# Kernel optimization log

Hardware: AMD Instinct MI355X
Metric: run time of the kernel (lower is better)

The kernel has to match this reference:

```python
import jax, jax.numpy as jnp
import numpy as np

C = 256
NH = 8
STRIDE = 4
HD = C // NH
SCALE = HD ** -0.5


def conv2d(x, w, b, stride=1, padding='VALID', groups=1):
    y = jax.lax.conv_general_dilated(
        x, w, (stride, stride), padding,
        dimension_numbers=('NCHW', 'OIHW', 'NCHW'),
        feature_group_count=groups)
    return y + b[None, :, None, None]


def setup_inputs() -> dict:
    key = jax.random.key(0)
    ks = jax.random.split(key, 20)
    s = 0.02
    d = {
        'x': jax.random.normal(ks[0], (8, C, 64, 64), jnp.float32),
        'wq': jax.random.normal(ks[1], (2 * C, C, 1, 1), jnp.float32) * s,
        'bq': jnp.zeros((2 * C,), jnp.float32),
        'ws': jax.random.normal(ks[2], (C, C, STRIDE, STRIDE), jnp.float32) * s,
        'bs': jnp.zeros((C,), jnp.float32),
        'wak_d': jax.random.normal(ks[3], (C, 1, 3, 3), jnp.float32) * s,
        'bak_d': jnp.zeros((C,), jnp.float32),
        'wak_p': jax.random.normal(ks[4], (C, C, 1, 1), jnp.float32) * s,
        'bak_p': jnp.zeros((C,), jnp.float32),
        'wav_d': jax.random.normal(ks[5], (C, 1, 3, 3), jnp.float32) * s,
        'bav_d': jnp.zeros((C,), jnp.float32),
        'wav_p': jax.random.normal(ks[6], (C, C, 1, 1), jnp.float32) * s,
        'bav_p': jnp.zeros((C,), jnp.float32),
        'wek': jax.random.normal(ks[7], (C, C, 1, 1), jnp.float32) * s,
        'bek': jnp.zeros((C,), jnp.float32),
        'wev': jax.random.normal(ks[8], (C, C, 1, 1), jnp.float32) * s,
        'bev': jnp.zeros((C,), jnp.float32),
        'wproj': jax.random.normal(ks[9], (C, 2 * C, 1, 1), jnp.float32) * s,
        'bproj': jnp.zeros((C,), jnp.float32),
    }
    return d


def _heads_kv(t):
    # [B,C,h,w] -> [B,NH,N_kv,HD]
    B = t.shape[0]
    return t.reshape(B, NH, HD, -1).transpose(0, 1, 3, 2)


def _attn_branch(q, k, v):
    # q: [B,NH,Nq,HD], k/v: [B,NH,Nkv,HD]
    attn = jnp.einsum('bhqd,bhkd->bhqk', q, k) * SCALE
    attn = jax.nn.softmax(attn, axis=-1)
    return jnp.einsum('bhqk,bhkd->bhqd', attn, v)


def reference(x, wq, bq, ws, bs, wak_d, bak_d, wak_p, bak_p,
              wav_d, bav_d, wav_p, bav_p, wek, bek, wev, bev, wproj, bproj):
    B, Cc, H, W = x.shape
    # QKV-style 1x1 query projection -> two query sets
    q = conv2d(x, wq, bq)  # [B,2C,H,W]
    q = q.reshape(B, 2, NH, HD, H * W).transpose(1, 0, 2, 4, 3)  # [2,B,NH,HW,HD]
    qa, qe = q[0], q[1]
    # spatial reduction
    xr = conv2d(x, ws, bs, stride=STRIDE)  # [B,C,H/s,W/s]
    spak = _heads_kv(conv2d(conv2d(xr, wak_d, bak_d, padding=[(1, 1), (1, 1)], groups=C), wak_p, bak_p))
    spav = _heads_kv(conv2d(conv2d(xr, wav_d, bav_d, padding=[(1, 1), (1, 1)], groups=C), wav_p, bav_p))
    spek = _heads_kv(conv2d(xr, wek, bek))
    spev = _heads_kv(conv2d(xr, wev, bev))
    outa = _attn_branch(qa, spak, spav).transpose(0, 1, 3, 2).reshape(B, Cc, H, W)
    oute = _attn_branch(qe, spek, spev).transpose(0, 1, 3, 2).reshape(B, Cc, H, W)
    out = jnp.concatenate((outa, oute), axis=1)
    return conv2d(out, wproj, bproj)
```

## Files before the change

### kernel.cpp

```cpp
#include <hip/hip_runtime.h>
#include <hip/hip_bf16.h>

#define QSC (0.17677669529663687f * 1.4426950408889634f)

typedef __attribute__((ext_vector_type(8))) short bf16x8;
typedef __attribute__((ext_vector_type(4))) float f32x4;
typedef unsigned short u16;

union FragU { unsigned u[4]; uint4 q; bf16x8 v; };

__device__ inline u16 f2bu(float a) {
  union { __hip_bfloat16 h; u16 s; } c;
  c.h = __float2bfloat16(a);
  return c.s;
}
__device__ inline unsigned pk2(float lo, float hi) {
  unsigned r;
  asm("v_cvt_pk_bf16_f32 %0, %1, %2" : "=v"(r) : "v"(lo), "v"(hi));
  return r;
}
__device__ inline float exp2r(float x) {
  float r;
  asm("v_exp_f32 %0, %1" : "=v"(r) : "v"(x));
  return r;
}
__device__ inline void gl16(const u16* g, u16* l) {
  __builtin_amdgcn_global_load_lds(
      (const __attribute__((address_space(1))) unsigned int*)g,
      (__attribute__((address_space(3))) unsigned int*)l, 16, 0, 0);
}
__device__ inline void waitvm0() {
  asm volatile("s_waitcnt vmcnt(0)" ::: "memory");
}

__global__ __launch_bounds__(256) void k_xT(
    const float* __restrict__ X, u16* __restrict__ XT,
    const float* __restrict__ wq, const float* __restrict__ wproj,
    const float* __restrict__ ws,
    const float* __restrict__ w0, const float* __restrict__ w1,
    const float* __restrict__ w2, const float* __restrict__ w3,
    u16* __restrict__ wqb, u16* __restrict__ wpb,
    u16* __restrict__ wsb, u16* __restrict__ wkvb) {
  if (blockIdx.z == 8) {
    int which = blockIdx.y;
    int tid = blockIdx.x * 256 + threadIdx.x;
    const int ST = 16384;
    if (which == 0) {
      for (int i = tid; i < 131072; i += ST) wqb[i] = f2bu(wq[i]);
    } else if (which == 1) {
      for (int i = tid; i < 131072; i += ST) wpb[i] = f2bu(wproj[i]);
    } else if (which == 2) {
      for (int i = tid; i < 1048576; i += ST) {
        int co = i >> 12, rem = i & 4095, tap = rem >> 8, ci = rem & 255;
        wsb[i] = f2bu(ws[co * 4096 + ci * 16 + tap]);
      }
    } else if (which < 7) {
      const float* src = (which == 3) ? w0 : (which == 4) ? w1 : (which == 5) ? w2 : w3;
      u16* dst = wkvb + (size_t)(which - 3) * 65536;
      for (int i = tid; i < 65536; i += ST) dst[i] = f2bu(src[i]);
    }
    return;
  }
  __shared__ float L[32 * 65];
  int n0 = blockIdx.x * 64, c0 = blockIdx.y * 32, b = blockIdx.z;
  int t = threadIdx.x;
#pragma unroll
  for (int i = 0; i < 8; ++i) {
    int idx = i * 256 + t;
    int r = idx >> 6, nn = idx & 63;
    L[r * 65 + nn] = X[((size_t)(b * 256 + c0 + r)) * 4096 + n0 + nn];
  }
  __syncthreads();
  int nn = t >> 2, cq = t & 3;
  uint4 u;
  u.x = pk2(L[(cq * 8 + 0) * 65 + nn], L[(cq * 8 + 1) * 65 + nn]);
  u.y = pk2(L[(cq * 8 + 2) * 65 + nn], L[(cq * 8 + 3) * 65 + nn]);
  u.z = pk2(L[(cq * 8 + 4) * 65 + nn], L[(cq * 8 + 5) * 65 + nn]);
  u.w = pk2(L[(cq * 8 + 6) * 65 + nn], L[(cq * 8 + 7) * 65 + nn]);
  *(uint4*)(XT + ((size_t)b * 4096 + n0 + nn) * 256 + c0 + cq * 8) = u;
}

__global__ __launch_bounds__(256) void k_gemm_qproj(
    const u16* __restrict__ XT, const u16* __restrict__ Wb,
    const float* __restrict__ bias, u16* __restrict__ Qb) {
  __shared__ __align__(16) u16 SM[16384];
  int n0 = blockIdx.x * 128, m0 = blockIdx.y * 128, b = blockIdx.z;
  int t = threadIdx.x, w = t >> 6, l = t & 63, g = l >> 4, lq = l & 15;
  int wr = w >> 1, wc = w & 1;
  const u16* Xb = XT + (size_t)b * 4096 * 256;
  int srow = w * 32 + (l >> 2), scol = (l & 3) * 8;
  const u16* gA = Wb + (size_t)(m0 + srow) * 256 + scol;
  const u16* gB = Xb + (size_t)(n0 + srow) * 256 + scol;
  u16* lA = SM + w * 1024;
  u16* lB = SM + 8192 + w * 1024;

  f32x4 acc[4][4];
#pragma unroll
  for (int ms = 0; ms < 4; ++ms)
#pragma unroll
    for (int ns = 0; ns < 4; ++ns) acc[ms][ns] = {0.f, 0.f, 0.f, 0.f};

  gl16(gA, lA); gl16(gA + 16 * 256, lA + 512);
  gl16(gB, lB); gl16(gB + 16 * 256, lB + 512);
  waitvm0();
  __syncthreads();
#pragma unroll
  for (int kt = 0; kt < 8; ++kt) {
    int cur = kt & 1;
    if (kt < 7) {
      int sel = cur ^ 1, ko = (kt + 1) * 32;
      gl16(gA + ko, lA + sel * 4096); gl16(gA + 16 * 256 + ko, lA + sel * 4096 + 512);
      gl16(gB + ko, lB + sel * 4096); gl16(gB + 16 * 256 + ko, lB + sel * 4096 + 512);
    }
    const u16* Ab = SM + cur * 4096;
    const u16* Bb = SM + 8192 + cur * 4096;
    FragU a[4], bb[4];
#pragma unroll
    for (int ms = 0; ms < 4; ++ms)
      a[ms].q = *(const uint4*)(Ab + (wr * 64 + ms * 16 + lq) * 32 + g * 8);
#pragma unroll
    for (int ns = 0; ns < 4; ++ns)
      bb[ns].q = *(const uint4*)(Bb + (wc * 64 + ns * 16 + lq) * 32 + g * 8);
#pragma unroll
    for (int ms = 0; ms < 4; ++ms)
#pragma unroll
      for (int ns = 0; ns < 4; ++ns)
        acc[ms][ns] = __builtin_amdgcn_mfma_f32_16x16x32_bf16(a[ms].v, bb[ns].v, acc[ms][ns], 0, 0, 0);
    waitvm0();
    __syncthreads();
  }

  float bR[4][4];
#pragma unroll
  for (int ms = 0; ms < 4; ++ms)
#pragma unroll
    for (int r = 0; r < 4; ++r) bR[ms][r] = bias[m0 + wr * 64 + ms * 16 + g * 4 + r];

  char* Lc = (char*)SM;
#pragma unroll
  for (int ms = 0; ms < 4; ++ms)
#pragma unroll
    for (int ns = 0; ns < 4; ++ns) {
      int nl = wc * 64 + ns * 16 + lq;
      int mb2 = (wr * 64 + ms * 16 + g * 4) * 2;
      int off = (nl * 256 + mb2) ^ ((nl & 7) << 4);
      *(uint2*)(Lc + off) = make_uint2(
          pk2((acc[ms][ns][0] + bR[ms][0]) * QSC, (acc[ms][ns][1] + bR[ms][1]) * QSC),
          pk2((acc[ms][ns][2] + bR[ms][2]) * QSC, (acc[ms][ns][3] + bR[ms][3]) * QSC));
    }
  __syncthreads();
  int sh0 = m0 >> 5;
#pragma unroll
  for (int rr = 0; rr < 8; ++rr) {
    int idx = rr * 256 + t;
    int ch = idx & 3, shl = (idx >> 2) & 3, nn = idx >> 4;
    int off = (nn * 256 + shl * 64 + ch * 16) ^ ((nn & 7) << 4);
    uint4 v = *(const uint4*)(Lc + off);
    *(uint4*)(Qb + ((size_t)(b * 16 + sh0 + shl) * 4096 + n0 + nn) * 32 + ch * 8) = v;
  }
}

__global__ __launch_bounds__(256) void k_gemm_sr(
    const u16* __restrict__ XT, const u16* __restrict__ Wb,
    float* __restrict__ Psr) {
  __shared__ __align__(16) u16 SM[16384];
  int ks = blockIdx.x, b = blockIdx.z;
  int m0 = (blockIdx.y >> 1) * 128, n0 = (blockIdx.y & 1) * 128;
  int t = threadIdx.x, w = t >> 6, l = t & 63, g = l >> 4, lq = l & 15;
  int wr = w >> 1, wc = w & 1;
  const u16* Xb = XT + (size_t)b * 4096 * 256;
  int srow = w * 32 + (l >> 2), scol = (l & 3) * 8;
  const u16* gA = Wb + (size_t)(m0 + srow) * 4096 + scol;
  u16* lA = SM + w * 1024;
  u16* lB = SM + 8192 + w * 1024;
  int nA = n0 + srow, nB = nA + 16;
  int iA = nA >> 4, jA = nA & 15, iB = nB >> 4, jB = nB & 15;

  f32x4 acc[4][4];
#pragma unroll
  for (int ms = 0; ms < 4; ++ms)
#pragma unroll
    for (int ns = 0; ns < 4; ++ns) acc[ms][ns] = {0.f, 0.f, 0.f, 0.f};

#define SR_STAGE(sel, kt) {                                                   \
    int ktg = ks * 16 + (kt);                                                 \
    int tap = ktg >> 3, ci0 = (ktg & 7) * 32;                                 \
    int ky = tap >> 2, kx = tap & 3;                                          \
    gl16(gA + ktg * 32, lA + (sel) * 4096);                                   \
    gl16(gA + (size_t)16 * 4096 + ktg * 32, lA + (sel) * 4096 + 512);         \
    int pixA = (4 * iA + ky) * 64 + 4 * jA + kx;                              \
    int pixB = (4 * iB + ky) * 64 + 4 * jB + kx;                              \
    gl16(Xb + (size_t)pixA * 256 + ci0 + scol, lB + (sel) * 4096);            \
    gl16(Xb + (size_t)pixB * 256 + ci0 + scol, lB + (sel) * 4096 + 512); }

  SR_STAGE(0, 0);
  waitvm0();
  __syncthreads();
#pragma unroll
  for (int kt = 0; kt < 16; ++kt) {
    int cur = kt & 1;
    if (kt < 15) SR_STAGE(cur ^ 1, kt + 1);
    const u16* Ab = SM + cur * 4096;
    const u16* Bb = SM + 8192 + cur * 4096;
    FragU a[4], bb[4];
#pragma unroll
    for (int ms = 0; ms < 4; ++ms)
      a[ms].q = *(const uint4*)(Ab + (wr * 64 + ms * 16 + lq) * 32 + g * 8);
#pragma unroll
    for (int ns = 0; ns < 4; ++ns)
      bb[ns].q = *(const uint4*)(Bb + (wc * 64 + ns * 16 + lq) * 32 + g * 8);
#pragma unroll
    for (int ms = 0; ms < 4; ++ms)
#pragma unroll
      for (int ns = 0; ns < 4; ++ns)
        acc[ms][ns] = __builtin_amdgcn_mfma_f32_16x16x32_bf16(a[ms].v, bb[ns].v, acc[ms][ns], 0, 0, 0);
    waitvm0();
    __syncthreads();
  }
#undef SR_STAGE
#pragma unroll
  for (int ms = 0; ms < 4; ++ms)
#pragma unroll
    for (int ns = 0; ns < 4; ++ns) {
      int n = n0 + wc * 64 + ns * 16 + lq;
#pragma unroll
      for (int r = 0; r < 4; ++r) {
        int m = m0 + wr * 64 + ms * 16 + g * 4 + r;
        Psr[(((size_t)ks * 8 + b) * 256 + m) * 256 + n] = acc[ms][ns][r];
      }
    }
}

__global__ __launch_bounds__(256) void k_srdw(
    const float* __restrict__ Psr, const float* __restrict__ bias,
    const float* __restrict__ wkd, const float* __restrict__ bkd,
    const float* __restrict__ wvd, const float* __restrict__ bvd,
    u16* __restrict__ xrT, u16* __restrict__ TKt, u16* __restrict__ TVt) {
  __shared__ float L[32 * 256];
  int cg = blockIdx.x, b = blockIdx.y, t = threadIdx.x;
#pragma unroll
  for (int r = 0; r < 32; ++r) {
    int c = cg * 32 + r;
    float s = bias[c];
#pragma unroll
    for (int ks = 0; ks < 8; ++ks)
      s += Psr[(((size_t)ks * 8 + b) * 256 + c) * 256 + t];
    L[r * 256 + t] = s;
  }
  __syncthreads();
  {
    unsigned wv[16];
#pragma unroll
    for (int r2 = 0; r2 < 16; ++r2)
      wv[r2] = pk2(L[(2 * r2) * 256 + t], L[(2 * r2 + 1) * 256 + t]);
    u16* dst = xrT + ((size_t)b * 256 + t) * 256 + cg * 32;
    *(uint4*)(dst + 0)  = make_uint4(wv[0], wv[1], wv[2], wv[3]);
    *(uint4*)(dst + 8)  = make_uint4(wv[4], wv[5], wv[6], wv[7]);
    *(uint4*)(dst + 16) = make_uint4(wv[8], wv[9], wv[10], wv[11]);
    *(uint4*)(dst + 24) = make_uint4(wv[12], wv[13], wv[14], wv[15]);
  }
  int i = t >> 4, j = t & 15;
  unsigned wk[16], wvv[16];
#pragma unroll
  for (int r2 = 0; r2 < 16; ++r2) {
    int c0 = cg * 32 + 2 * r2;
    float ak0 = bkd[c0], ak1 = bkd[c0 + 1];
    float av0 = bvd[c0], av1 = bvd[c0 + 1];
#pragma unroll
    for (int ky = 0; ky < 3; ++ky) {
      int ii = i + ky - 1;
      if (ii < 0 || ii > 15) continue;
#pragma unroll
      for (int kx = 0; kx < 3; ++kx) {
        int jj = j + kx - 1;
        if (jj < 0 || jj > 15) continue;
        float v0 = L[(2 * r2) * 256 + ii * 16 + jj];
        float v1 = L[(2 * r2 + 1) * 256 + ii * 16 + jj];
        float wk0 = wkd[c0 * 9 + ky * 3 + kx], wk1 = wkd[(c0 + 1) * 9 + ky * 3 + kx];
        float wv0 = wvd[c0 * 9 + ky * 3 + kx], wv1 = wvd[(c0 + 1) * 9 + ky * 3 + kx];
        ak0 = fmaf(v0, wk0, ak0); ak1 = fmaf(v1, wk1, ak1);
        av0 = fmaf(v0, wv0, av0); av1 = fmaf(v1, wv1, av1);
      }
    }
    wk[r2] = pk2(ak0, ak1);
    wvv[r2] = pk2(av0, av1);
  }
  u16* dk = TKt + ((size_t)b * 256 + t) * 256 + cg * 32;
  u16* dv = TVt + ((size_t)b * 256 + t) * 256 + cg * 32;
  *(uint4*)(dk + 0)  = make_uint4(wk[0], wk[1], wk[2], wk[3]);
  *(uint4*)(dk + 8)  = make_uint4(wk[4], wk[5], wk[6], wk[7]);
  *(uint4*)(dk + 16) = make_uint4(wk[8], wk[9], wk[10], wk[11]);
  *(uint4*)(dk + 24) = make_uint4(wk[12], wk[13], wk[14], wk[15]);
  *(uint4*)(dv + 0)  = make_uint4(wvv[0], wvv[1], wvv[2], wvv[3]);
  *(uint4*)(dv + 8)  = make_uint4(wvv[4], wvv[5], wvv[6], wvv[7]);
  *(uint4*)(dv + 16) = make_uint4(wvv[8], wvv[9], wvv[10], wvv[11]);
  *(uint4*)(dv + 24) = make_uint4(wvv[12], wvv[13], wvv[14], wvv[15]);
}

__global__ __launch_bounds__(256) void k_gemm_kv(
    const u16* __restrict__ xrT, const u16* __restrict__ tkT, const u16* __restrict__ tvT,
    const u16* __restrict__ wkvb,
    const float* __restrict__ bak_p, const float* __restrict__ bav_p,
    const float* __restrict__ bek, const float* __restrict__ bev,
    u16* __restrict__ KV) {
  int which = blockIdx.x, m0 = blockIdx.y * 64, b = blockIdx.z;
  const u16* XT; const float* bias;
  if (which == 0)      { XT = tkT; bias = bak_p; }
  else if (which == 1) { XT = tvT; bias = bav_p; }
  else if (which == 2) { XT = xrT; bias = bek; }
  else                 { XT = xrT; bias = bev; }
  const u16* Wb = wkvb + (size_t)which * 65536;
  int t = threadIdx.x, w = t >> 6, l = t & 63, g = l >> 4, lq = l & 15;
  const u16* Xb = XT + (size_t)b * 65536;
  char* img = (char*)(KV + (size_t)(which * 64 + b * 8) * 8192);
  f32x4 acc[4][4];
#pragma unroll
  for (int ms = 0; ms < 4; ++ms)
#pragma unroll
    for (int ns = 0; ns < 4; ++ns) acc[ms][ns] = {0.f, 0.f, 0.f, 0.f};

  if (!(which & 1)) {
#pragma unroll
    for (int k0 = 0; k0 < 256; k0 += 32) {
      FragU a[4], bb[4];
#pragma unroll
      for (int ms = 0; ms < 4; ++ms)
        a[ms].q = *(const uint4*)(Wb + (size_t)(m0 + ms * 16 + lq) * 256 + k0 + g * 8);
#pragma unroll
      for (int ns = 0; ns < 4; ++ns)
        bb[ns].q = *(const uint4*)(Xb + (size_t)(w * 64 + ns * 16 + lq) * 256 + k0 + g * 8);
#pragma unroll
      for (int ms = 0; ms < 4; ++ms)
#pragma unroll
        for (int ns = 0; ns < 4; ++ns)
          acc[ms][ns] = __builtin_amdgcn_mfma_f32_16x16x32_bf16(a[ms].v, bb[ns].v, acc[ms][ns], 0, 0, 0);
    }
    float bR[4][4];
#pragma unroll
    for (int ms = 0; ms < 4; ++ms)
#pragma unroll
      for (int r = 0; r < 4; ++r) bR[ms][r] = bias[m0 + ms * 16 + g * 4 + r];
#pragma unroll
    for (int ms = 0; ms < 4; ++ms) {
      int mm = m0 + ms * 16 + g * 4;
      int h = mm >> 5, d0 = mm & 31;
      int cb = (d0 >> 3) * 16, e0 = (d0 & 7) * 2;
#pragma unroll
      for (int ns = 0; ns < 4; ++ns) {
        int n = w * 64 + ns * 16 + lq;
        int off = ((n * 64 + cb) ^ (((n >> 1) & 7) << 4)) + e0;
        *(uint2*)(img + (size_t)h * 16384 + off) =
            make_uint2(pk2(acc[ms][ns][0] + bR[ms][0], acc[ms][ns][1] + bR[ms][1]),
                       pk2(acc[ms][ns][2] + bR[ms][2], acc[ms][ns][3] + bR[ms][3]));
      }
    }
  } else {
#pragma unroll
    for (int k0 = 0; k0 < 256; k0 += 32) {
      FragU a[4], bb[4];
#pragma unroll
      for (int ms = 0; ms < 4; ++ms)
        a[ms].q = *(const uint4*)(Wb + (size_t)(m0 + ms * 16 + lq) * 256 + k0 + g * 8);
#pragma unroll
      for (int ns = 0; ns < 4; ++ns)
        bb[ns].q = *(const uint4*)(Xb + (size_t)(w * 64 + ns * 16 + lq) * 256 + k0 + g * 8);
#pragma unroll
      for (int ms = 0; ms < 4; ++ms)
#pragma unroll
        for (int ns = 0; ns < 4; ++ns)
          acc[ms][ns] = __builtin_amdgcn_mfma_f32_16x16x32_bf16(bb[ns].v, a[ms].v, acc[ms][ns], 0, 0, 0);
    }
    float bR[4];
#pragma unroll
    for (int ms = 0; ms < 4; ++ms) bR[ms] = bias[m0 + ms * 16 + lq];
#pragma unroll
    for (int ms = 0; ms < 4; ++ms) {
      int mm = m0 + ms * 16 + lq;
      int h = mm >> 5, d = mm & 31;
      int rowb = d * 512, swz = ((d >> 1) & 7) << 4;
#pragma unroll
      for (int ns = 0; ns < 4; ++ns) {
        int nn = w * 64 + ns * 16 + g * 4;
        int off = (rowb + nn * 2) ^ swz;
        *(uint2*)(img + (size_t)h * 16384 + off) =
            make_uint2(pk2(acc[ms][ns][0] + bR[ms], acc[ms][ns][1] + bR[ms]),
                       pk2(acc[ms][ns][2] + bR[ms], acc[ms][ns][3] + bR[ms]));
      }
    }
  }
}

__global__ __launch_bounds__(256) void k_attn_mfma(
    const u16* __restrict__ Qb, const u16* __restrict__ KV,
    u16* __restrict__ ObT) {
  int h = blockIdx.y, z = blockIdx.z;
  int set = z >> 3, b = z & 7;
  __shared__ __align__(16) u16 Ks[8192];
  __shared__ __align__(16) u16 Vt[8192];
  int t = threadIdx.x;
  {
    const uint4* kg = (const uint4*)(KV + ((size_t)((set * 2 + 0) * 64 + b * 8 + h)) * 8192);
    const uint4* vg = (const uint4*)(KV + ((size_t)((set * 2 + 1) * 64 + b * 8 + h)) * 8192);
    uint4* kd = (uint4*)Ks;
    uint4* vd = (uint4*)Vt;
#pragma unroll
    for (int i = 0; i < 4; ++i) {
      kd[i * 256 + t] = kg[i * 256 + t];
      vd[i * 256 + t] = vg[i * 256 + t];
    }
  }
  __syncthreads();

  int w = t >> 6, l = t & 63;
  int lq = l & 15, g = l >> 4;
  int n0 = (blockIdx.x << 7) + w * 32;

  FragU qfA, qfB;
  const u16* qrow = Qb + ((size_t)(b * 16 + set * 8 + h) * 4096 + n0 + lq) * 32 + g * 8;
  qfA.q = *(const uint4*)(qrow);
  qfB.q = *(const uint4*)(qrow + 16 * 32);

  int aA = lq >> 2, cC = lq & 3;
  int lbK = ((aA << 9) + (cC << 6) + (g << 4)) ^ ((cC >> 1) << 4) ^ ((aA & 1) << 6);
  const char* pe = (const char*)Ks + lbK;
  const char* po = (const char*)Ks + ((lbK ^ 32) + 256);

  unsigned pkuA[32], pkuB[32];
#pragma unroll
  for (int k2 = 0; k2 < 8; ++k2) {
    FragU af;
    f32x4 cA, cB;
    af.q = *(const uint4*)(pe + k2 * 2048);
    cA = {0.f, 0.f, 0.f, 0.f};
    cA = __builtin_amdgcn_mfma_f32_16x16x32_bf16(af.v, qfA.v, cA, 0, 0, 0);
    cB = {0.f, 0.f, 0.f, 0.f};
    cB = __builtin_amdgcn_mfma_f32_16x16x32_bf16(af.v, qfB.v, cB, 0, 0, 0);
    pkuA[4 * k2 + 0] = pk2(exp2r(cA[0]), exp2r(cA[1]));
    pkuA[4 * k2 + 1] = pk2(exp2r(cA[2]), exp2r(cA[3]));
    pkuB[4 * k2 + 0] = pk2(exp2r(cB[0]), exp2r(cB[1]));
    pkuB[4 * k2 + 1] = pk2(exp2r(cB[2]), exp2r(cB[3]));
    af.q = *(const uint4*)(po + k2 * 2048);
    cA = {0.f, 0.f, 0.f, 0.f};
    cA = __builtin_amdgcn_mfma_f32_16x16x32_bf16(af.v, qfA.v, cA, 0, 0, 0);
    cB = {0.f, 0.f, 0.f, 0.f};
    cB = __builtin_amdgcn_mfma_f32_16x16x32_bf16(af.v, qfB.v, cB, 0, 0, 0);
    pkuA[4 * k2 + 2] = pk2(exp2r(cA[0]), exp2r(cA[1]));
    pkuA[4 * k2 + 3] = pk2(exp2r(cA[2]), exp2r(cA[3]));
    pkuB[4 * k2 + 2] = pk2(exp2r(cB[0]), exp2r(cB[1]));
    pkuB[4 * k2 + 3] = pk2(exp2r(cB[2]), exp2r(cB[3]));
  }
  __syncthreads();

  int lbV = (lq << 9) + ((g << 4) ^ ((lq & 6) << 3));
  int kb = (lq >> 3) & 1;
  const char* pp = (const char*)Vt + (lbV + kb * 64);
  const char* pm = (const char*)Vt + (lbV - kb * 64);

  FragU ones;
  ones.u[0] = ones.u[1] = ones.u[2] = ones.u[3] = 0x3F803F80u;
  f32x4 oA0 = {0.f, 0.f, 0.f, 0.f}, oA1 = {0.f, 0.f, 0.f, 0.f};
  f32x4 oB0 = {0.f, 0.f, 0.f, 0.f}, oB1 = {0.f, 0.f, 0.f, 0.f};
  f32x4 saA = {0.f, 0.f, 0.f, 0.f}, saB = {0.f, 0.f, 0.f, 0.f};
#pragma unroll
  for (int kv = 0; kv < 8; ++kv) {
    FragU pbA, pbB;
    pbA.u[0] = pkuA[4 * kv + 0]; pbA.u[1] = pkuA[4 * kv + 1];
    pbA.u[2] = pkuA[4 * kv + 2]; pbA.u[3] = pkuA[4 * kv + 3];
    pbB.u[0] = pkuB[4 * kv + 0]; pbB.u[1] = pkuB[4 * kv + 1];
    pbB.u[2] = pkuB[4 * kv + 2]; pbB.u[3] = pkuB[4 * kv + 3];
    const char* pv = (kv & 1) ? pm : pp;
    FragU va0, va1;
    va0.q = *(const uint4*)(pv + kv * 64);
    va1.q = *(const uint4*)(pv + kv * 64 + 8192);
    oA0 = __builtin_amdgcn_mfma_f32_16x16x32_bf16(va0.v, pbA.v, oA0, 0, 0, 0);
    oA1 = __builtin_amdgcn_mfma_f32_16x16x32_bf16(va1.v, pbA.v, oA1, 0, 0, 0);
    oB0 = __builtin_amdgcn_mfma_f32_16x16x32_bf16(va0.v, pbB.v, oB0, 0, 0, 0);
    oB1 = __builtin_amdgcn_mfma_f32_16x16x32_bf16(va1.v, pbB.v, oB1, 0, 0, 0);
    saA = __builtin_amdgcn_mfma_f32_16x16x32_bf16(ones.v, pbA.v, saA, 0, 0, 0);
    saB = __builtin_amdgcn_mfma_f32_16x16x32_bf16(ones.v, pbB.v, saB, 0, 0, 0);
  }

  float invA = __builtin_amdgcn_rcpf(saA[0]);
  float invB = __builtin_amdgcn_rcpf(saB[0]);
  {
    char* ob = (char*)Ks;
    int nnA = w * 32 + lq, nnB = nnA + 16;
    *(uint2*)(ob + nnA * 80 + g * 8) =
        make_uint2(pk2(oA0[0] * invA, oA0[1] * invA), pk2(oA0[2] * invA, oA0[3] * invA));
    *(uint2*)(ob + nnA * 80 + 32 + g * 8) =
        make_uint2(pk2(oA1[0] * invA, oA1[1] * invA), pk2(oA1[2] * invA, oA1[3] * invA));
    *(uint2*)(ob + nnB * 80 + g * 8) =
        make_uint2(pk2(oB0[0] * invB, oB0[1] * invB), pk2(oB0[2] * invB, oB0[3] * invB));
    *(uint2*)(ob + nnB * 80 + 32 + g * 8) =
        make_uint2(pk2(oB1[0] * invB, oB1[1] * invB), pk2(oB1[2] * invB, oB1[3] * invB));
  }
  __syncthreads();
#pragma unroll
  for (int rep = 0; rep < 2; ++rep) {
    int idx = rep * 256 + t;
    int nn = idx >> 2, dq = idx & 3;
    uint4 v = *(const uint4*)((const char*)Ks + nn * 80 + dq * 16);
    *(uint4*)(ObT + ((size_t)b * 4096 + (blockIdx.x << 7) + nn) * 512 +
              set * 256 + h * 32 + dq * 8) = v;
  }
}

__global__ __launch_bounds__(256) void k_gemm_proj(
    const u16* __restrict__ XT, const u16* __restrict__ Wb,
    const float* __restrict__ bias, float* __restrict__ Y) {
  __shared__ __align__(16) u16 SM[16384];
  int n0 = blockIdx.x * 128, m0 = blockIdx.y * 128, b = blockIdx.z;
  int t = threadIdx.x, w = t >> 6, l = t & 63, g = l >> 4, lq = l & 15;
  int wr = w >> 1, wc = w & 1;
  const u16* Xb = XT + (size_t)b * 4096 * 512;
  int srow = w * 32 + (l >> 2), scol = (l & 3) * 8;
  const u16* gA = Wb + (size_t)(m0 + srow) * 512 + scol;
  const u16* gB = Xb + (size_t)(n0 + srow) * 512 + scol;
  u16* lA = SM + w * 1024;
  u16* lB = SM + 8192 + w * 1024;

  f32x4 acc[4][4];
#pragma unroll
  for (int ms = 0; ms < 4; ++ms)
#pragma unroll
    for (int ns = 0; ns < 4; ++ns) acc[ms][ns] = {0.f, 0.f, 0.f, 0.f};

  gl16(gA, lA); gl16(gA + 16 * 512, lA + 512);
  gl16(gB, lB); gl16(gB + 16 * 512, lB + 512);
  waitvm0();
  __syncthreads();
#pragma unroll
  for (int kt = 0; kt < 16; ++kt) {
    int cur = kt & 1;
    if (kt < 15) {
      int sel = cur ^ 1, ko = (kt + 1) * 32;
      gl16(gA + ko, lA + sel * 4096); gl16(gA + 16 * 512 + ko, lA + sel * 4096 + 512);
      gl16(gB + ko, lB + sel * 4096); gl16(gB + 16 * 512 + ko, lB + sel * 4096 + 512);
    }
    const u16* Ab = SM + cur * 4096;
    const u16* Bb = SM + 8192 + cur * 4096;
    FragU a[4], bb[4];
#pragma unroll
    for (int ms = 0; ms < 4; ++ms)
      a[ms].q = *(const uint4*)(Ab + (wr * 64 + ms * 16 + lq) * 32 + g * 8);
#pragma unroll
    for (int ns = 0; ns < 4; ++ns)
      bb[ns].q = *(const uint4*)(Bb + (wc * 64 + ns * 16 + lq) * 32 + g * 8);
#pragma unroll
    for (int ms = 0; ms < 4; ++ms)
#pragma unroll
      for (int ns = 0; ns < 4; ++ns)
        acc[ms][ns] = __builtin_amdgcn_mfma_f32_16x16x32_bf16(a[ms].v, bb[ns].v, acc[ms][ns], 0, 0, 0);
    waitvm0();
    __syncthreads();
  }
#pragma unroll
  for (int ms = 0; ms < 4; ++ms)
#pragma unroll
    for (int ns = 0; ns < 4; ++ns) {
      int n = n0 + wc * 64 + ns * 16 + lq;
#pragma unroll
      for (int r = 0; r < 4; ++r) {
        int m = m0 + wr * 64 + ms * 16 + g * 4 + r;
        Y[((size_t)b * 256 + m) * 4096 + n] = acc[ms][ns][r] + bias[m];
      }
    }
}


extern "C" void kernel_launch(void* const* d_in, const int* in_sizes, int n_in,
                              void* d_out, int out_size, void* d_ws, size_t ws_size,
                              hipStream_t stream) {
  (void)in_sizes; (void)n_in; (void)out_size; (void)ws_size;
  const float* x     = (const float*)d_in[0];
  const float* wq    = (const float*)d_in[1];
  const float* bq    = (const float*)d_in[2];
  const float* wsw   = (const float*)d_in[3];
  const float* bs    = (const float*)d_in[4];
  const float* wak_d = (const float*)d_in[5];
  const float* bak_d = (const float*)d_in[6];
  const float* wak_p = (const float*)d_in[7];
  const float* bak_p = (const float*)d_in[8];
  const float* wav_d = (const float*)d_in[9];
  const float* bav_d = (const float*)d_in[10];
  const float* wav_p = (const float*)d_in[11];
  const float* bav_p = (const float*)d_in[12];
  const float* wek   = (const float*)d_in[13];
  const float* bek   = (const float*)d_in[14];
  const float* wev   = (const float*)d_in[15];
  const float* bev   = (const float*)d_in[16];
  const float* wproj = (const float*)d_in[17];
  const float* bproj = (const float*)d_in[18];
  float* out = (float*)d_out;

  char* p = (char*)d_ws;
  u16* xbT  = (u16*)p;   p += (size_t)8 * 4096 * 256 * 2;
  u16* qb   = (u16*)p;   p += (size_t)8 * 16 * 4096 * 32 * 2;
  u16* obT  = (u16*)p;   p += (size_t)8 * 4096 * 512 * 2;
  float* psr = (float*)p; p += (size_t)8 * 8 * 256 * 256 * 4;
  u16* xrT  = (u16*)p;   p += (size_t)524288 * 2;
  u16* tkT  = (u16*)p;   p += (size_t)524288 * 2;
  u16* tvT  = (u16*)p;   p += (size_t)524288 * 2;
  u16* kvimg = (u16*)p;  p += (size_t)4 * 64 * 8192 * 2;
  u16* wqb  = (u16*)p;   p += (size_t)131072 * 2;
  u16* wpb  = (u16*)p;   p += (size_t)131072 * 2;
  u16* wsb  = (u16*)p;   p += (size_t)1048576 * 2;
  u16* wkvb = (u16*)p;   p += (size_t)262144 * 2;

  k_xT<<<dim3(64, 8, 9), 256, 0, stream>>>(x, xbT, wq, wproj, wsw,
                                           wak_p, wav_p, wek, wev,
                                           wqb, wpb, wsb, wkvb);
  k_gemm_qproj<<<dim3(32, 4, 8), 256, 0, stream>>>(xbT, wqb, bq, qb);
  k_gemm_sr<<<dim3(8, 4, 8), 256, 0, stream>>>(xbT, wsb, psr);
  k_srdw<<<dim3(8, 8), 256, 0, stream>>>(psr, bs, wak_d, bak_d, wav_d, bav_d,
                                         xrT, tkT, tvT);
  k_gemm_kv<<<dim3(4, 4, 8), 256, 0, stream>>>(xrT, tkT, tvT, wkvb,
                                               bak_p, bav_p, bek, bev, kvimg);
  k_attn_mfma<<<dim3(32, 8, 16), 256, 0, stream>>>(qb, kvimg, obT);
  k_gemm_proj<<<dim3(32, 2, 8), 256, 0, stream>>>(obT, wpb, bproj, out);
}
```

Before: 142.1 us.

## Merge q-projection and spatial-reduction GEMMs, split srdw finer, tune attention

Combines the query-projection GEMM and the strided spatial-reduction GEMM into one launch that dispatches on blockIdx.x, so both share one grid and the small SR work overlaps with the larger GEMM. Halves the channel group per block in the depthwise/reduction kernel to launch twice as many blocks. In attention, K/V tiles are now staged with direct global-to-LDS loads, and s_setprio is raised around MFMA sections. These remove a launch and improve occupancy, but the combined kernel may have a larger register footprint and imbalanced block durations.

```diff
diff --git a/kernel.cpp b/kernel.cpp
--- a/kernel.cpp
+++ b/kernel.cpp
@@ -80,17 +80,16 @@
   *(uint4*)(XT + ((size_t)b * 4096 + n0 + nn) * 256 + c0 + cq * 8) = u;
 }
 
-__global__ __launch_bounds__(256) void k_gemm_qproj(
-    const u16* __restrict__ XT, const u16* __restrict__ Wb,
-    const float* __restrict__ bias, u16* __restrict__ Qb) {
+__global__ __launch_bounds__(256) void k_gemm_x(
+    const u16* __restrict__ XT, const u16* __restrict__ Wqb,
+    const float* __restrict__ bias, u16* __restrict__ Qb,
+    const u16* __restrict__ Wsb, float* __restrict__ Psr) {
   __shared__ __align__(16) u16 SM[16384];
-  int n0 = blockIdx.x * 128, m0 = blockIdx.y * 128, b = blockIdx.z;
+  int b = blockIdx.z;
   int t = threadIdx.x, w = t >> 6, l = t & 63, g = l >> 4, lq = l & 15;
   int wr = w >> 1, wc = w & 1;
   const u16* Xb = XT + (size_t)b * 4096 * 256;
   int srow = w * 32 + (l >> 2), scol = (l & 3) * 8;
-  const u16* gA = Wb + (size_t)(m0 + srow) * 256 + scol;
-  const u16* gB = Xb + (size_t)(n0 + srow) * 256 + scol;
   u16* lA = SM + w * 1024;
   u16* lB = SM + 8192 + w * 1024;
 
@@ -100,87 +99,75 @@
 #pragma unroll
     for (int ns = 0; ns < 4; ++ns) acc[ms][ns] = {0.f, 0.f, 0.f, 0.f};
 
-  gl16(gA, lA); gl16(gA + 16 * 256, lA + 512);
-  gl16(gB, lB); gl16(gB + 16 * 256, lB + 512);
-  waitvm0();
-  __syncthreads();
-#pragma unroll
-  for (int kt = 0; kt < 8; ++kt) {
-    int cur = kt & 1;
-    if (kt < 7) {
-      int sel = cur ^ 1, ko = (kt + 1) * 32;
-      gl16(gA + ko, lA + sel * 4096); gl16(gA + 16 * 256 + ko, lA + sel * 4096 + 512);
-      gl16(gB + ko, lB + sel * 4096); gl16(gB + 16 * 256 + ko, lB + sel * 4096 + 512);
-    }
-    const u16* Ab = SM + cur * 4096;
-    const u16* Bb = SM + 8192 + cur * 4096;
-    FragU a[4], bb[4];
-#pragma unroll
-    for (int ms = 0; ms < 4; ++ms)
-      a[ms].q = *(const uint4*)(Ab + (wr * 64 + ms * 16 + lq) * 32 + g * 8);
-#pragma unroll
-    for (int ns = 0; ns < 4; ++ns)
-      bb[ns].q = *(const uint4*)(Bb + (wc * 64 + ns * 16 + lq) * 32 + g * 8);
-#pragma unroll
-    for (int ms = 0; ms < 4; ++ms)
-#pragma unroll
-      for (int ns = 0; ns < 4; ++ns)
-        acc[ms][ns] = __builtin_amdgcn_mfma_f32_16x16x32_bf16(a[ms].v, bb[ns].v, acc[ms][ns], 0, 0, 0);
+  if (blockIdx.x < 32) {
+    int n0 = blockIdx.x * 128, m0 = blockIdx.y * 128;
+    const u16* gA = Wqb + (size_t)(m0 + srow) * 256 + scol;
+    const u16* gB = Xb + (size_t)(n0 + srow) * 256 + scol;
+
+    gl16(gA, lA); gl16(gA + 16 * 256, lA + 512);
+    gl16(gB, lB); gl16(gB + 16 * 256, lB + 512);
     waitvm0();
     __syncthreads();
-  }
-
-  float bR[4][4];
-#pragma unroll
-  for (int ms = 0; ms < 4; ++ms)
-#pragma unroll
-    for (int r = 0; r < 4; ++r) bR[ms][r] = bias[m0 + wr * 64 + ms * 16 + g * 4 + r];
-
-  char* Lc = (char*)SM;
-#pragma unroll
-  for (int ms = 0; ms < 4; ++ms)
-#pragma unroll
-    for (int ns = 0; ns < 4; ++ns) {
-      int nl = wc * 64 + ns * 16 + lq;
-      int mb2 = (wr * 64 + ms * 16 + g * 4) * 2;
-      int off = (nl * 256 + mb2) ^ ((nl & 7) << 4);
-      *(uint2*)(Lc + off) = make_uint2(
-          pk2((acc[ms][ns][0] + bR[ms][0]) * QSC, (acc[ms][ns][1] + bR[ms][1]) * QSC),
-          pk2((acc[ms][ns][2] + bR[ms][2]) * QSC, (acc[ms][ns][3] + bR[ms][3]) * QSC));
-    }
-  __syncthreads();
-  int sh0 = m0 >> 5;
-#pragma unroll
-  for (int rr = 0; rr < 8; ++rr) {
-    int idx = rr * 256 + t;
-    int ch = idx & 3, shl = (idx >> 2) & 3, nn = idx >> 4;
-    int off = (nn * 256 + shl * 64 + ch * 16) ^ ((nn & 7) << 4);
-    uint4 v = *(const uint4*)(Lc + off);
-    *(uint4*)(Qb + ((size_t)(b * 16 + sh0 + shl) * 4096 + n0 + nn) * 32 + ch * 8) = v;
-  }
-}
-
-__global__ __launch_bounds__(256) void k_gemm_sr(
-    const u16* __restrict__ XT, const u16* __restrict__ Wb,
-    float* __restrict__ Psr) {
-  __shared__ __align__(16) u16 SM[16384];
-  int ks = blockIdx.x, b = blockIdx.z;
-  int m0 = (blockIdx.y >> 1) * 128, n0 = (blockIdx.y & 1) * 128;
-  int t = threadIdx.x, w = t >> 6, l = t & 63, g = l >> 4, lq = l & 15;
-  int wr = w >> 1, wc = w & 1;
-  const u16* Xb = XT + (size_t)b * 4096 * 256;
-  int srow = w * 32 + (l >> 2), scol = (l & 3) * 8;
-  const u16* gA = Wb + (size_t)(m0 + srow) * 4096 + scol;
-  u16* lA = SM + w * 1024;
-  u16* lB = SM + 8192 + w * 1024;
-  int nA = n0 + srow, nB = nA + 16;
-  int iA = nA >> 4, jA = nA & 15, iB = nB >> 4, jB = nB & 15;
-
-  f32x4 acc[4][4];
-#pragma unroll
-  for (int ms = 0; ms < 4; ++ms)
-#pragma unroll
-    for (int ns = 0; ns < 4; ++ns) acc[ms][ns] = {0.f, 0.f, 0.f, 0.f};
+#pragma unroll
+    for (int kt = 0; kt < 8; ++kt) {
+      int cur = kt & 1;
+      if (kt < 7) {
+        int sel = cur ^ 1, ko = (kt + 1) * 32;
+        gl16(gA + ko, lA + sel * 4096); gl16(gA + 16 * 256 + ko, lA + sel * 4096 + 512);
+        gl16(gB + ko, lB + sel * 4096); gl16(gB + 16 * 256 + ko, lB + sel * 4096 + 512);
+      }
+      const u16* Ab = SM + cur * 4096;
+      const u16* Bb = SM + 8192 + cur * 4096;
+      FragU a[4], bb[4];
+#pragma unroll
+      for (int ms = 0; ms < 4; ++ms)
+        a[ms].q = *(const uint4*)(Ab + (wr * 64 + ms * 16 + lq) * 32 + g * 8);
+#pragma unroll
+      for (int ns = 0; ns < 4; ++ns)
+        bb[ns].q = *(const uint4*)(Bb + (wc * 64 + ns * 16 + lq) * 32 + g * 8);
+#pragma unroll
+      for (int ms = 0; ms < 4; ++ms)
+#pragma unroll
+        for (int ns = 0; ns < 4; ++ns)
+          acc[ms][ns] = __builtin_amdgcn_mfma_f32_16x16x32_bf16(a[ms].v, bb[ns].v, acc[ms][ns], 0, 0, 0);
+      waitvm0();
+      __syncthreads();
+    }
+
+    float bR[4][4];
+#pragma unroll
+    for (int ms = 0; ms < 4; ++ms)
+#pragma unroll
+      for (int r = 0; r < 4; ++r) bR[ms][r] = bias[m0 + wr * 64 + ms * 16 + g * 4 + r];
+
+    char* Lc = (char*)SM;
+#pragma unroll
+    for (int ms = 0; ms < 4; ++ms)
+#pragma unroll
+      for (int ns = 0; ns < 4; ++ns) {
+        int nl = wc * 64 + ns * 16 + lq;
+        int mb2 = (wr * 64 + ms * 16 + g * 4) * 2;
+        int off = (nl * 256 + mb2) ^ ((nl & 7) << 4);
+        *(uint2*)(Lc + off) = make_uint2(
+            pk2((acc[ms][ns][0] + bR[ms][0]) * QSC, (acc[ms][ns][1] + bR[ms][1]) * QSC),
+            pk2((acc[ms][ns][2] + bR[ms][2]) * QSC, (acc[ms][ns][3] + bR[ms][3]) * QSC));
+      }
+    __syncthreads();
+    int sh0 = m0 >> 5;
+#pragma unroll
+    for (int rr = 0; rr < 8; ++rr) {
+      int idx = rr * 256 + t;
+      int ch = idx & 3, shl = (idx >> 2) & 3, nn = idx >> 4;
+      int off = (nn * 256 + shl * 64 + ch * 16) ^ ((nn & 7) << 4);
+      uint4 v = *(const uint4*)(Lc + off);
+      *(uint4*)(Qb + ((size_t)(b * 16 + sh0 + shl) * 4096 + n0 + nn) * 32 + ch * 8) = v;
+    }
+  } else {
+    int ks = blockIdx.x - 32;
+    int m0 = (blockIdx.y >> 1) * 128, n0 = (blockIdx.y & 1) * 128;
+    const u16* gA = Wsb + (size_t)(m0 + srow) * 4096 + scol;
+    int nA = n0 + srow, nB = nA + 16;
+    int iA = nA >> 4, jA = nA & 15, iB = nB >> 4, jB = nB & 15;
 
 #define SR_STAGE(sel, kt) {                                                   \
     int ktg = ks * 16 + (kt);                                                 \
@@ -193,42 +180,43 @@
     gl16(Xb + (size_t)pixA * 256 + ci0 + scol, lB + (sel) * 4096);            \
     gl16(Xb + (size_t)pixB * 256 + ci0 + scol, lB + (sel) * 4096 + 512); }
 
-  SR_STAGE(0, 0);
-  waitvm0();
-  __syncthreads();
-#pragma unroll
-  for (int kt = 0; kt < 16; ++kt) {
-    int cur = kt & 1;
-    if (kt < 15) SR_STAGE(cur ^ 1, kt + 1);
-    const u16* Ab = SM + cur * 4096;
-    const u16* Bb = SM + 8192 + cur * 4096;
-    FragU a[4], bb[4];
-#pragma unroll
-    for (int ms = 0; ms < 4; ++ms)
-      a[ms].q = *(const uint4*)(Ab + (wr * 64 + ms * 16 + lq) * 32 + g * 8);
-#pragma unroll
-    for (int ns = 0; ns < 4; ++ns)
-      bb[ns].q = *(const uint4*)(Bb + (wc * 64 + ns * 16 + lq) * 32 + g * 8);
-#pragma unroll
-    for (int ms = 0; ms < 4; ++ms)
-#pragma unroll
-      for (int ns = 0; ns < 4; ++ns)
-        acc[ms][ns] = __builtin_amdgcn_mfma_f32_16x16x32_bf16(a[ms].v, bb[ns].v, acc[ms][ns], 0, 0, 0);
+    SR_STAGE(0, 0);
     waitvm0();
     __syncthreads();
-  }
+#pragma unroll
+    for (int kt = 0; kt < 16; ++kt) {
+      int cur = kt & 1;
+      if (kt < 15) SR_STAGE(cur ^ 1, kt + 1);
+      const u16* Ab = SM + cur * 4096;
+      const u16* Bb = SM + 8192 + cur * 4096;
+      FragU a[4], bb[4];
+#pragma unroll
+      for (int ms = 0; ms < 4; ++ms)
+        a[ms].q = *(const uint4*)(Ab + (wr * 64 + ms * 16 + lq) * 32 + g * 8);
+#pragma unroll
+      for (int ns = 0; ns < 4; ++ns)
+        bb[ns].q = *(const uint4*)(Bb + (wc * 64 + ns * 16 + lq) * 32 + g * 8);
+#pragma unroll
+      for (int ms = 0; ms < 4; ++ms)
+#pragma unroll
+        for (int ns = 0; ns < 4; ++ns)
+          acc[ms][ns] = __builtin_amdgcn_mfma_f32_16x16x32_bf16(a[ms].v, bb[ns].v, acc[ms][ns], 0, 0, 0);
+      waitvm0();
+      __syncthreads();
+    }
 #undef SR_STAGE
 #pragma unroll
-  for (int ms = 0; ms < 4; ++ms)
-#pragma unroll
-    for (int ns = 0; ns < 4; ++ns) {
-      int n = n0 + wc * 64 + ns * 16 + lq;
-#pragma unroll
-      for (int r = 0; r < 4; ++r) {
-        int m = m0 + wr * 64 + ms * 16 + g * 4 + r;
-        Psr[(((size_t)ks * 8 + b) * 256 + m) * 256 + n] = acc[ms][ns][r];
-      }
-    }
+    for (int ms = 0; ms < 4; ++ms)
+#pragma unroll
+      for (int ns = 0; ns < 4; ++ns) {
+        int n = n0 + wc * 64 + ns * 16 + lq;
+#pragma unroll
+        for (int r = 0; r < 4; ++r) {
+          int m = m0 + wr * 64 + ms * 16 + g * 4 + r;
+          Psr[(((size_t)ks * 8 + b) * 256 + m) * 256 + n] = acc[ms][ns][r];
+        }
+      }
+  }
 }
 
 __global__ __launch_bounds__(256) void k_srdw(
@@ -236,11 +224,11 @@
     const float* __restrict__ wkd, const float* __restrict__ bkd,
     const float* __restrict__ wvd, const float* __restrict__ bvd,
     u16* __restrict__ xrT, u16* __restrict__ TKt, u16* __restrict__ TVt) {
-  __shared__ float L[32 * 256];
+  __shared__ float L[16 * 256];
   int cg = blockIdx.x, b = blockIdx.y, t = threadIdx.x;
 #pragma unroll
-  for (int r = 0; r < 32; ++r) {
-    int c = cg * 32 + r;
+  for (int r = 0; r < 16; ++r) {
+    int c = cg * 16 + r;
     float s = bias[c];
 #pragma unroll
     for (int ks = 0; ks < 8; ++ks)
@@ -249,21 +237,19 @@
   }
   __syncthreads();
   {
-    unsigned wv[16];
-#pragma unroll
-    for (int r2 = 0; r2 < 16; ++r2)
+    unsigned wv[8];
+#pragma unroll
+    for (int r2 = 0; r2 < 8; ++r2)
       wv[r2] = pk2(L[(2 * r2) * 256 + t], L[(2 * r2 + 1) * 256 + t]);
-    u16* dst = xrT + ((size_t)b * 256 + t) * 256 + cg * 32;
-    *(uint4*)(dst + 0)  = make_uint4(wv[0], wv[1], wv[2], wv[3]);
-    *(uint4*)(dst + 8)  = make_uint4(wv[4], wv[5], wv[6], wv[7]);
-    *(uint4*)(dst + 16) = make_uint4(wv[8], wv[9], wv[10], wv[11]);
-    *(uint4*)(dst + 24) = make_uint4(wv[12], wv[13], wv[14], wv[15]);
+    u16* dst = xrT + ((size_t)b * 256 + t) * 256 + cg * 16;
+    *(uint4*)(dst + 0) = make_uint4(wv[0], wv[1], wv[2], wv[3]);
+    *(uint4*)(dst + 8) = make_uint4(wv[4], wv[5], wv[6], wv[7]);
   }
   int i = t >> 4, j = t & 15;
-  unsigned wk[16], wvv[16];
-#pragma unroll
-  for (int r2 = 0; r2 < 16; ++r2) {
-    int c0 = cg * 32 + 2 * r2;
+  unsigned wk[8], wvv[8];
+#pragma unroll
+  for (int r2 = 0; r2 < 8; ++r2) {
+    int c0 = cg * 16 + 2 * r2;
     float ak0 = bkd[c0], ak1 = bkd[c0 + 1];
     float av0 = bvd[c0], av1 = bvd[c0 + 1];
 #pragma unroll
@@ -285,16 +271,12 @@
     wk[r2] = pk2(ak0, ak1);
     wvv[r2] = pk2(av0, av1);
   }
-  u16* dk = TKt + ((size_t)b * 256 + t) * 256 + cg * 32;
-  u16* dv = TVt + ((size_t)b * 256 + t) * 256 + cg * 32;
-  *(uint4*)(dk + 0)  = make_uint4(wk[0], wk[1], wk[2], wk[3]);
-  *(uint4*)(dk + 8)  = make_uint4(wk[4], wk[5], wk[6], wk[7]);
-  *(uint4*)(dk + 16) = make_uint4(wk[8], wk[9], wk[10], wk[11]);
-  *(uint4*)(dk + 24) = make_uint4(wk[12], wk[13], wk[14], wk[15]);
-  *(uint4*)(dv + 0)  = make_uint4(wvv[0], wvv[1], wvv[2], wvv[3]);
-  *(uint4*)(dv + 8)  = make_uint4(wvv[4], wvv[5], wvv[6], wvv[7]);
-  *(uint4*)(dv + 16) = make_uint4(wvv[8], wvv[9], wvv[10], wvv[11]);
-  *(uint4*)(dv + 24) = make_uint4(wvv[12], wvv[13], wvv[14], wvv[15]);
+  u16* dk = TKt + ((size_t)b * 256 + t) * 256 + cg * 16;
+  u16* dv = TVt + ((size_t)b * 256 + t) * 256 + cg * 16;
+  *(uint4*)(dk + 0) = make_uint4(wk[0], wk[1], wk[2], wk[3]);
+  *(uint4*)(dk + 8) = make_uint4(wk[4], wk[5], wk[6], wk[7]);
+  *(uint4*)(dv + 0) = make_uint4(wvv[0], wvv[1], wvv[2], wvv[3]);
+  *(uint4*)(dv + 8) = make_uint4(wvv[4], wvv[5], wvv[6], wvv[7]);
 }
 
 __global__ __launch_bounds__(256) void k_gemm_kv(
@@ -397,21 +379,19 @@
   int set = z >> 3, b = z & 7;
   __shared__ __align__(16) u16 Ks[8192];
   __shared__ __align__(16) u16 Vt[8192];
-  int t = threadIdx.x;
+  int t = threadIdx.x, w = t >> 6, l = t & 63;
   {
-    const uint4* kg = (const uint4*)(KV + ((size_t)((set * 2 + 0) * 64 + b * 8 + h)) * 8192);
-    const uint4* vg = (const uint4*)(KV + ((size_t)((set * 2 + 1) * 64 + b * 8 + h)) * 8192);
-    uint4* kd = (uint4*)Ks;
-    uint4* vd = (uint4*)Vt;
+    const u16* kg = KV + (size_t)((set * 2 + 0) * 64 + b * 8 + h) * 8192;
+    const u16* vg = KV + (size_t)((set * 2 + 1) * 64 + b * 8 + h) * 8192;
 #pragma unroll
     for (int i = 0; i < 4; ++i) {
-      kd[i * 256 + t] = kg[i * 256 + t];
-      vd[i * 256 + t] = vg[i * 256 + t];
-    }
+      gl16(kg + w * 2048 + i * 512 + l * 8, Ks + w * 2048 + i * 512);
+      gl16(vg + w * 2048 + i * 512 + l * 8, Vt + w * 2048 + i * 512);
+    }
+    waitvm0();
   }
   __syncthreads();
 
-  int w = t >> 6, l = t & 63;
   int lq = l & 15, g = l >> 4;
   int n0 = (blockIdx.x << 7) + w * 32;
 
@@ -431,19 +411,23 @@
     FragU af;
     f32x4 cA, cB;
     af.q = *(const uint4*)(pe + k2 * 2048);
+    __builtin_amdgcn_s_setprio(1);
     cA = {0.f, 0.f, 0.f, 0.f};
     cA = __builtin_amdgcn_mfma_f32_16x16x32_bf16(af.v, qfA.v, cA, 0, 0, 0);
     cB = {0.f, 0.f, 0.f, 0.f};
     cB = __builtin_amdgcn_mfma_f32_16x16x32_bf16(af.v, qfB.v, cB, 0, 0, 0);
+    __builtin_amdgcn_s_setprio(0);
     pkuA[4 * k2 + 0] = pk2(exp2r(cA[0]), exp2r(cA[1]));
     pkuA[4 * k2 + 1] = pk2(exp2r(cA[2]), exp2r(cA[3]));
     pkuB[4 * k2 + 0] = pk2(exp2r(cB[0]), exp2r(cB[1]));
     pkuB[4 * k2 + 1] = pk2(exp2r(cB[2]), exp2r(cB[3]));
     af.q = *(const uint4*)(po + k2 * 2048);
+    __builtin_amdgcn_s_setprio(1);
     cA = {0.f, 0.f, 0.f, 0.f};
     cA = __builtin_amdgcn_mfma_f32_16x16x32_bf16(af.v, qfA.v, cA, 0, 0, 0);
     cB = {0.f, 0.f, 0.f, 0.f};
     cB = __builtin_amdgcn_mfma_f32_16x16x32_bf16(af.v, qfB.v, cB, 0, 0, 0);
+    __builtin_amdgcn_s_setprio(0);
     pkuA[4 * k2 + 2] = pk2(exp2r(cA[0]), exp2r(cA[1]));
     pkuA[4 * k2 + 3] = pk2(exp2r(cA[2]), exp2r(cA[3]));
     pkuB[4 * k2 + 2] = pk2(exp2r(cB[0]), exp2r(cB[1]));
@@ -461,6 +445,7 @@
   f32x4 oA0 = {0.f, 0.f, 0.f, 0.f}, oA1 = {0.f, 0.f, 0.f, 0.f};
   f32x4 oB0 = {0.f, 0.f, 0.f, 0.f}, oB1 = {0.f, 0.f, 0.f, 0.f};
   f32x4 saA = {0.f, 0.f, 0.f, 0.f}, saB = {0.f, 0.f, 0.f, 0.f};
+  __builtin_amdgcn_s_setprio(1);
 #pragma unroll
   for (int kv = 0; kv < 8; ++kv) {
     FragU pbA, pbB;
@@ -479,6 +464,7 @@
     saA = __builtin_amdgcn_mfma_f32_16x16x32_bf16(ones.v, pbA.v, saA, 0, 0, 0);
     saB = __builtin_amdgcn_mfma_f32_16x16x32_bf16(ones.v, pbB.v, saB, 0, 0, 0);
   }
+  __builtin_amdgcn_s_setprio(0);
 
   float invA = __builtin_amdgcn_rcpf(saA[0]);
   float invB = __builtin_amdgcn_rcpf(saB[0]);
@@ -610,10 +596,9 @@
   k_xT<<<dim3(64, 8, 9), 256, 0, stream>>>(x, xbT, wq, wproj, wsw,
                                            wak_p, wav_p, wek, wev,
                                            wqb, wpb, wsb, wkvb);
-  k_gemm_qproj<<<dim3(32, 4, 8), 256, 0, stream>>>(xbT, wqb, bq, qb);
-  k_gemm_sr<<<dim3(8, 4, 8), 256, 0, stream>>>(xbT, wsb, psr);
-  k_srdw<<<dim3(8, 8), 256, 0, stream>>>(psr, bs, wak_d, bak_d, wav_d, bav_d,
-                                         xrT, tkT, tvT);
+  k_gemm_x<<<dim3(40, 4, 8), 256, 0, stream>>>(xbT, wqb, bq, qb, wsb, psr);
+  k_srdw<<<dim3(16, 8), 256, 0, stream>>>(psr, bs, wak_d, bak_d, wav_d, bav_d,
+                                          xrT, tkT, tvT);
   k_gemm_kv<<<dim3(4, 4, 8), 256, 0, stream>>>(xrT, tkT, tvT, wkvb,
                                                bak_p, bav_p, bek, bev, kvimg);
   k_attn_mfma<<<dim3(32, 8, 16), 256, 0, stream>>>(qb, kvimg, obT);
```

Result: faster. 122.5 us (-13.8%).
